# Performance work log

Hardware: AMD Instinct MI355X
Metric: run time of the kernel (lower is better)

## Reference

```python
import jax, jax.numpy as jnp
import numpy as np

B, S, D, H = 4, 2048, 512, 8
HD = D // H


def rotate_half(t):
    half = t.shape[-1] // 2
    return jnp.concatenate([-t[..., half:], t[..., :half]], axis=-1)


def setup_inputs() -> dict:
    key = jax.random.key(0)
    ks = jax.random.split(key, 8)
    x = jax.random.normal(ks[0], (B, S, D), dtype=jnp.float32)
    # realistic rotary tables built from angles
    inv_freq = 1.0 / (10000.0 ** (jnp.arange(0, D // 2, dtype=jnp.float32) / (D // 2)))
    ang = jnp.arange(S, dtype=jnp.float32)[:, None] * inv_freq[None, :]  # [S, D/2]
    ang = jnp.concatenate([ang, ang], axis=-1)  # [S, D]
    cos_emb = jnp.cos(ang)[None]  # [1, S, D]
    sin_emb = jnp.sin(ang)[None]
    mask = jax.random.randint(ks[1], (B, S, S), 0, 2).astype(jnp.bool_)
    scale = 1.0 / np.sqrt(D)
    wq = jax.random.normal(ks[2], (D, D), dtype=jnp.float32) * scale
    wk = jax.random.normal(ks[3], (D, D), dtype=jnp.float32) * scale
    wv = jax.random.normal(ks[4], (D, D), dtype=jnp.float32) * scale
    wo = jax.random.normal(ks[5], (D, D), dtype=jnp.float32) * scale
    return {"x": x, "cos_emb": cos_emb, "sin_emb": sin_emb, "mask": mask,
            "wq": wq, "wk": wk, "wv": wv, "wo": wo}


def reference(x, cos_emb, sin_emb, mask, wq, wk, wv, wo):
    bsz, seqlen, dim = x.shape
    # projections (weights stored as [in, out])
    xq = x @ wq
    xk = x @ wk
    xv = x @ wv
    # RoPE applied over full dim before head split (as in original)
    xq = xq * cos_emb + rotate_half(xq) * sin_emb
    xk = xk * cos_emb + rotate_half(xk) * sin_emb
    # split heads: [B, H, S, HD]
    xq = xq.reshape(bsz, seqlen, H, HD).transpose(0, 2, 1, 3)
    xk = xk.reshape(bsz, seqlen, H, HD).transpose(0, 2, 1, 3)
    xv = xv.reshape(bsz, seqlen, H, HD).transpose(0, 2, 1, 3)
    scores = jnp.einsum('bhqd,bhkd->bhqk', xq, xk) / jnp.sqrt(jnp.float32(HD))
    scores = scores + (~mask)[:, None].astype(scores.dtype) * (-1e9)
    scores = jax.nn.softmax(scores.astype(jnp.float32), axis=-1).astype(xq.dtype)
    scores = scores * mask[:, None].astype(scores.dtype)
    out = jnp.einsum('bhqk,bhkd->bhqd', scores, xv)
    out = out.transpose(0, 2, 1, 3).reshape(bsz, seqlen, dim)
    return out @ wo
```

## Files before the change

kernel.cpp:

```cpp
#include <hip/hip_runtime.h>
#include <hip/hip_bf16.h>

typedef __bf16 bf16x8 __attribute__((ext_vector_type(8)));
typedef float f32x4 __attribute__((ext_vector_type(4)));
typedef short short8 __attribute__((ext_vector_type(8)));

#define MFMA16(a, b, c) __builtin_amdgcn_mfma_f32_16x16x32_bf16((a), (b), (c), 0, 0, 0)

static constexpr int S = 2048;
static constexpr int D = 512;
static constexpr int HD = 64;
static constexpr int KBLK = 64;
#define QSCALE 0.18033688011112042f

typedef __attribute__((address_space(1))) const unsigned int gu32;
typedef __attribute__((address_space(3))) unsigned int lu32;

__device__ __forceinline__ void gll16(const void* g, void* l) {
  __builtin_amdgcn_global_load_lds((gu32*)g, (lu32*)l, 16, 0, 0);
}

__device__ __forceinline__ unsigned short f2b(float f) {
  return __builtin_bit_cast(unsigned short, __float2bfloat16(f));
}
__device__ __forceinline__ float b2f(unsigned short u) {
  return __builtin_bit_cast(float, (unsigned)u << 16);
}

__global__ void maskbits_kernel(const int* __restrict__ m, unsigned long long* __restrict__ bits) {
  int gid = blockIdx.x * 256 + threadIdx.x;
  int lane = threadIdx.x & 63;
  unsigned long long w = __ballot(m[gid] != 0);
  if (lane == 0) bits[gid >> 6] = w;
}

__global__ void cast_x_kernel(const float* __restrict__ x, unsigned short* __restrict__ xb) {
  int idx = blockIdx.x * 256 + threadIdx.x;
  float4 v = ((const float4*)x)[idx];
  ushort4 o;
  o.x = f2b(v.x); o.y = f2b(v.y); o.z = f2b(v.z); o.w = f2b(v.w);
  ((ushort4*)xb)[idx] = o;
}

__global__ void wtrans4_kernel(const float* __restrict__ wq, const float* __restrict__ wk,
                               const float* __restrict__ wv, const float* __restrict__ wo,
                               unsigned short* __restrict__ wqkvT, unsigned short* __restrict__ woT) {
  __shared__ float t[64][65];
  const int z = blockIdx.z;
  const float* w = (z == 0) ? wq : (z == 1) ? wk : (z == 2) ? wv : wo;
  unsigned short* dst = (z < 3) ? wqkvT + (size_t)z * 512 * 512 : woT;
  const int i0 = blockIdx.x * 64, o0 = blockIdx.y * 64;
  for (int it = 0; it < 16; ++it) {
    int idx = it * 256 + threadIdx.x;
    int ii = idx >> 6, oo = idx & 63;
    t[oo][ii] = w[(size_t)(i0 + ii) * 512 + o0 + oo];
  }
  __syncthreads();
  for (int it = 0; it < 16; ++it) {
    int idx = it * 256 + threadIdx.x;
    int oo = idx >> 6, ii = idx & 63;
    dst[(size_t)(o0 + oo) * 512 + i0 + ii] = f2b(t[oo][ii]);
  }
}

__global__ __launch_bounds__(256)
void gemm2(const unsigned short* __restrict__ A, const unsigned short* __restrict__ Bt,
           int M, int N, int K, float* __restrict__ Cf,
           unsigned short* __restrict__ qd, unsigned short* __restrict__ kd,
           unsigned short* __restrict__ vtd, int mode) {
  __shared__ alignas(16) unsigned short lds[2][2][4096];
  const int tid = threadIdx.x;
  const int lane = tid & 63, l15 = lane & 15, lg = lane >> 4;
  const int wave = tid >> 6;
  const int m0 = blockIdx.x * 128, n0 = blockIdx.y * 128;
  const int wm = (wave >> 1) * 64, wn = (wave & 1) * 64;
  const int wbase = wave * 512;
  const int grow = tid >> 2, gcol = (tid & 3) * 8;
  f32x4 acc[4][4] = {};
  const int nt = K / 32;

#define GSTAGE(sb, kk)                                                              \
  do {                                                                              \
    gll16(&A[(size_t)(m0 + grow) * K + (kk) + gcol], &lds[sb][0][wbase]);           \
    gll16(&A[(size_t)(m0 + 64 + grow) * K + (kk) + gcol], &lds[sb][0][2048 + wbase]);\
    gll16(&Bt[(size_t)(n0 + grow) * K + (kk) + gcol], &lds[sb][1][wbase]);          \
    gll16(&Bt[(size_t)(n0 + 64 + grow) * K + (kk) + gcol], &lds[sb][1][2048 + wbase]);\
  } while (0)

  GSTAGE(0, 0);
  asm volatile("s_waitcnt vmcnt(0)" ::: "memory");
  __syncthreads();
  for (int t = 0; t < nt; ++t) {
    const int cur = t & 1;
    if (t + 1 < nt) GSTAGE(cur ^ 1, (t + 1) * 32);
    bf16x8 af[4], bfr[4];
#pragma unroll
    for (int i = 0; i < 4; ++i) {
      af[i]  = *(const bf16x8*)&lds[cur][0][(wm + i * 16 + l15) * 32 + lg * 8];
      bfr[i] = *(const bf16x8*)&lds[cur][1][(wn + i * 16 + l15) * 32 + lg * 8];
    }
    __builtin_amdgcn_s_setprio(1);
#pragma unroll
    for (int i = 0; i < 4; ++i)
#pragma unroll
      for (int j = 0; j < 4; ++j)
        acc[i][j] = MFMA16(af[i], bfr[j], acc[i][j]);
    __builtin_amdgcn_s_setprio(0);
    asm volatile("s_waitcnt vmcnt(0)" ::: "memory");
    __syncthreads();
  }
#undef GSTAGE

  if (mode == 0) {
#pragma unroll
    for (int i = 0; i < 4; ++i)
#pragma unroll
      for (int j = 0; j < 4; ++j)
#pragma unroll
        for (int r = 0; r < 4; ++r)
          Cf[(size_t)(m0 + wm + i * 16 + lg * 4 + r) * N + (n0 + wn + j * 16 + l15)] = acc[i][j][r];
  } else {
    const int sel = n0 >> 9;
    const int nb = (n0 & 511) + wn;
    if (sel < 2) {
      unsigned short* dst = (sel == 0) ? qd : kd;
#pragma unroll
      for (int i = 0; i < 4; ++i)
#pragma unroll
        for (int j = 0; j < 4; ++j)
#pragma unroll
          for (int r = 0; r < 4; ++r) {
            const int m = m0 + wm + i * 16 + lg * 4 + r;
            const int nn = nb + j * 16 + l15;
            dst[(((size_t)(m >> 11) * 8 + (nn >> 6)) * 2048 + (m & 2047)) * 64 + (nn & 63)] =
                f2b(acc[i][j][r]);
          }
    } else {
#pragma unroll
      for (int i = 0; i < 4; ++i)
#pragma unroll
        for (int j = 0; j < 4; ++j)
#pragma unroll
          for (int r = 0; r < 4; ++r) {
            const int m = m0 + wm + i * 16 + lg * 4 + r;
            const int nn = nb + j * 16 + l15;
            vtd[(((size_t)(m >> 11) * 8 + (nn >> 6)) * 64 + (nn & 63)) * 2048 + (m & 2047)] =
                f2b(acc[i][j][r]);
          }
    }
  }
}

__global__ void rope_pair_kernel(const unsigned short* __restrict__ qpre, const unsigned short* __restrict__ kpre,
                                 const float* __restrict__ cose, const float* __restrict__ sine,
                                 unsigned short* __restrict__ qb, unsigned short* __restrict__ kb) {
  const int idx = blockIdx.x * 256 + threadIdx.x;
  const int hd0 = (idx & 7) * 8;
  const int rr = idx >> 3;
  const int b = rr >> 13, h = (rr >> 11) & 3, s = rr & 2047;
  const size_t lo = ((size_t)(b * 8 + h) * 2048 + s) * 64 + hd0;
  const size_t hi = lo + (size_t)4 * 2048 * 64;
  const int d0 = h * 64 + hd0;
  short8 qlo = *(const short8*)&qpre[lo];
  short8 qhi = *(const short8*)&qpre[hi];
  short8 klo = *(const short8*)&kpre[lo];
  short8 khi = *(const short8*)&kpre[hi];
  float4 c0 = *(const float4*)&cose[(size_t)s * 512 + d0];
  float4 c1 = *(const float4*)&cose[(size_t)s * 512 + d0 + 4];
  float4 s0 = *(const float4*)&sine[(size_t)s * 512 + d0];
  float4 s1 = *(const float4*)&sine[(size_t)s * 512 + d0 + 4];
  float cc[8] = {c0.x, c0.y, c0.z, c0.w, c1.x, c1.y, c1.z, c1.w};
  float ss[8] = {s0.x, s0.y, s0.z, s0.w, s1.x, s1.y, s1.z, s1.w};
  short8 qolo, qohi, kolo, kohi;
#pragma unroll
  for (int j = 0; j < 8; ++j) {
    float ql = b2f((unsigned short)qlo[j]), qh = b2f((unsigned short)qhi[j]);
    float kl = b2f((unsigned short)klo[j]), kh = b2f((unsigned short)khi[j]);
    qolo[j] = (short)f2b((ql * cc[j] - qh * ss[j]) * QSCALE);
    qohi[j] = (short)f2b((qh * cc[j] + ql * ss[j]) * QSCALE);
    kolo[j] = (short)f2b(kl * cc[j] - kh * ss[j]);
    kohi[j] = (short)f2b(kh * cc[j] + kl * ss[j]);
  }
  *(short8*)&qb[lo] = qolo;
  *(short8*)&qb[hi] = qohi;
  *(short8*)&kb[lo] = kolo;
  *(short8*)&kb[hi] = kohi;
}

__global__ __launch_bounds__(512)
void flash_kernel(const unsigned short* __restrict__ qb, const unsigned short* __restrict__ kb,
                  const unsigned short* __restrict__ vtb, const unsigned long long* __restrict__ mbits,
                  float* __restrict__ op0, float* __restrict__ op1,
                  float* __restrict__ ls0, float* __restrict__ ls1) {
  __shared__ alignas(16) unsigned short kv[3][2][4096];
  __shared__ alignas(16) f32x4 btab[16];
  const int tid = threadIdx.x;
  const int wave = tid >> 6, lane = tid & 63;
  const int l15 = lane & 15, lg = lane >> 4;
  const int swz = (l15 & 7) << 4;
  const int wgid = blockIdx.x;
  const int slot = wgid >> 3;
  const int bh = (wgid & 7) * 4 + (slot & 3);
  const int rest = slot >> 2;
  const int kh = rest & 1;
  const int q0 = (rest >> 1) * 128 + wave * 16;
  const int b = bh >> 3, h = bh & 7;
  const int kbase = kh * 1024;
  const unsigned short* Q = qb + ((size_t)bh * S + q0) * HD;
  const unsigned short* Kp = kb + (size_t)bh * S * HD;
  const unsigned short* Vt = vtb + (size_t)bh * HD * S;
  const unsigned long long* Mrow = mbits + ((size_t)b * S + q0 + l15) * (S / 64) + kh * 16;
  float* opart = kh ? op1 : op0;
  float* lsum = kh ? ls1 : ls0;

  const int srow = tid >> 3;
  const int scol = ((tid & 7) ^ (srow & 7)) * 8;
  const int ksrow = ((srow & 15) >> 2) * 8 + ((srow >> 4) & 1) * 4 + (srow & 3) + (srow >> 5) * 32;
  const int wbase = wave * 512;

  if (tid < 16) {
    f32x4 e;
    e[0] = (tid & 1) ? 0.f : -300.f;
    e[1] = (tid & 2) ? 0.f : -300.f;
    e[2] = (tid & 4) ? 0.f : -300.f;
    e[3] = (tid & 8) ? 0.f : -300.f;
    btab[tid] = e;
  }

  bf16x8 qf0 = *(const bf16x8*)&Q[l15 * HD + lg * 8];
  bf16x8 qf1 = *(const bf16x8*)&Q[l15 * HD + 32 + lg * 8];
  f32x4 o[4] = {};
  float lpart = 0.f;
  const int lgs8 = lg * 8;

  unsigned long long wA = Mrow[0];
  gll16(&Kp[(size_t)(kbase + ksrow) * HD + scol], &kv[0][0][wbase]);
  gll16(&Vt[(size_t)srow * S + kbase + scol], &kv[0][1][wbase]);
  unsigned long long wB = Mrow[1];
  gll16(&Kp[(size_t)(kbase + 64 + ksrow) * HD + scol], &kv[1][0][wbase]);
  gll16(&Vt[(size_t)srow * S + kbase + 64 + scol], &kv[1][1][wbase]);
  asm volatile("s_waitcnt vmcnt(3) lgkmcnt(0)" ::: "memory");
  __builtin_amdgcn_s_barrier();

  int bi = 0;
  for (int t = 0; t < 16; ++t) {
    unsigned long long wC = 0;
    if (t + 2 < 16) {
      const int kn = kbase + (t + 2) * KBLK;
      const int bn = (bi == 0) ? 2 : bi - 1;
      wC = Mrow[t + 2];
      gll16(&Kp[(size_t)(kn + ksrow) * HD + scol], &kv[bn][0][wbase]);
      gll16(&Vt[(size_t)srow * S + kn + scol], &kv[bn][1][wbase]);
    }
    const char* kbp = (const char*)&kv[bi][0][0];
    const char* vbp = (const char*)&kv[bi][1][0];

    f32x4 sc[4] = {};
    __builtin_amdgcn_s_setprio(1);
#pragma unroll
    for (int n = 0; n < 4; ++n) {
      const int cb = (n * 16 + l15) * 128 + ((lg * 16) ^ swz);
      bf16x8 kf0 = *(const bf16x8*)(kbp + cb);
      bf16x8 kf1 = *(const bf16x8*)(kbp + (cb ^ 64));
      sc[n] = MFMA16(kf0, qf0, sc[n]);
      sc[n] = MFMA16(kf1, qf1, sc[n]);
    }
    __builtin_amdgcn_s_setprio(0);

    f32x4 pv[4];
    {
      const unsigned nib0 = (unsigned)(wA >> (lgs8 + 0)) & 15u;
      const unsigned nib1 = (unsigned)(wA >> (lgs8 + 4)) & 15u;
      const unsigned nib2 = (unsigned)(wA >> (lgs8 + 32)) & 15u;
      const unsigned nib3 = (unsigned)(wA >> (lgs8 + 36)) & 15u;
      const f32x4 b0 = btab[nib0], b1 = btab[nib1], b2 = btab[nib2], b3 = btab[nib3];
#pragma unroll
      for (int r = 0; r < 4; ++r) {
        pv[0][r] = __builtin_amdgcn_exp2f(sc[0][r] + b0[r]);
        pv[1][r] = __builtin_amdgcn_exp2f(sc[1][r] + b1[r]);
        pv[2][r] = __builtin_amdgcn_exp2f(sc[2][r] + b2[r]);
        pv[3][r] = __builtin_amdgcn_exp2f(sc[3][r] + b3[r]);
      }
    }
    f32x4 s4 = (pv[0] + pv[1]) + (pv[2] + pv[3]);
    lpart += (s4[0] + s4[1]) + (s4[2] + s4[3]);

    bf16x8 pf0, pf1;
#pragma unroll
    for (int j = 0; j < 4; ++j) {
      pf0[j]     = (__bf16)pv[0][j];
      pf0[j + 4] = (__bf16)pv[1][j];
      pf1[j]     = (__bf16)pv[2][j];
      pf1[j + 4] = (__bf16)pv[3][j];
    }

    __builtin_amdgcn_s_setprio(1);
#pragma unroll
    for (int n = 0; n < 4; ++n) {
      const int cb = (n * 16 + l15) * 128 + ((lg * 16) ^ swz);
      bf16x8 vf0 = *(const bf16x8*)(vbp + cb);
      bf16x8 vf1 = *(const bf16x8*)(vbp + (cb ^ 64));
      o[n] = MFMA16(pf0, vf0, o[n]);
      o[n] = MFMA16(pf1, vf1, o[n]);
    }
    __builtin_amdgcn_s_setprio(0);

    if (t < 14) { asm volatile("s_waitcnt vmcnt(3)" ::: "memory"); }
    else        { asm volatile("s_waitcnt vmcnt(0)" ::: "memory"); }
    __builtin_amdgcn_s_barrier();
    wA = wB; wB = wC;
    bi = (bi == 2) ? 0 : bi + 1;
  }

  lpart += __shfl_xor(lpart, 16);
  lpart += __shfl_xor(lpart, 32);
  if (lg == 0) lsum[(size_t)bh * S + q0 + l15] = lpart;
#pragma unroll
  for (int r = 0; r < 4; ++r)
#pragma unroll
    for (int n = 0; n < 4; ++n)
      opart[((size_t)(b * S + q0 + lg * 4 + r)) * D + h * HD + n * 16 + l15] = o[n][r];
}

__global__ __launch_bounds__(256)
void gemm_fused(const float* __restrict__ op0, const float* __restrict__ op1,
                const float* __restrict__ ls0, const float* __restrict__ ls1,
                const unsigned short* __restrict__ Bt, float* __restrict__ C) {
  __shared__ alignas(16) unsigned short ldsA[2][2048];
  __shared__ alignas(16) unsigned short ldsB[2][4096];
  __shared__ float invt[512];
  const int tid = threadIdx.x;
  const int lane = tid & 63, l15 = lane & 15, lg = lane >> 4;
  const int wave = tid >> 6;
  const int m0 = blockIdx.x * 64, n0 = blockIdx.y * 128;
  const int wm = (wave >> 1) * 32, wn = (wave & 1) * 64;
  const int wbase = wave * 512;
  const int grow = tid >> 2, gcol = (tid & 3) * 8;
  const int arow = m0 + (tid >> 2);
  const size_t abase = (size_t)arow * 512 + (tid & 3) * 8;
  f32x4 acc[2][4] = {};

  for (int e = tid; e < 512; e += 256) {
    const int row = e >> 3, hh = e & 7;
    const int m = m0 + row;
    const size_t li = ((size_t)((m >> 11) * 8 + hh)) * 2048 + (m & 2047);
    const float l = ls0[li] + ls1[li];
    invt[e] = (l > 0.f) ? 1.f / l : 0.f;
  }

#define BSTAGE(sb, kk)                                                               \
  do {                                                                               \
    gll16(&Bt[(size_t)(n0 + grow) * 512 + (kk) + gcol], &ldsB[sb][wbase]);           \
    gll16(&Bt[(size_t)(n0 + 64 + grow) * 512 + (kk) + gcol], &ldsB[sb][2048 + wbase]);\
  } while (0)

  float4 a0, a1, p0, p1;
#define ALOAD(kk)                                          \
  do {                                                     \
    a0 = *(const float4*)&op0[abase + (kk)];               \
    a1 = *(const float4*)&op0[abase + (kk) + 4];           \
    p0 = *(const float4*)&op1[abase + (kk)];               \
    p1 = *(const float4*)&op1[abase + (kk) + 4];           \
  } while (0)

#define AWRITE(sb, kk)                                                       \
  do {                                                                       \
    const float inv = invt[((tid >> 2) << 3) | ((kk) >> 6)];                 \
    short8 pk;                                                               \
    pk[0] = (short)f2b((a0.x + p0.x) * inv);                                 \
    pk[1] = (short)f2b((a0.y + p0.y) * inv);                                 \
    pk[2] = (short)f2b((a0.z + p0.z) * inv);                                 \
    pk[3] = (short)f2b((a0.w + p0.w) * inv);                                 \
    pk[4] = (short)f2b((a1.x + p1.x) * inv);                                 \
    pk[5] = (short)f2b((a1.y + p1.y) * inv);                                 \
    pk[6] = (short)f2b((a1.z + p1.z) * inv);                                 \
    pk[7] = (short)f2b((a1.w + p1.w) * inv);                                 \
    *(short8*)&ldsA[sb][(tid >> 2) * 32 + (tid & 3) * 8] = pk;               \
  } while (0)

  ALOAD(0);
  BSTAGE(0, 0);
  __syncthreads();
  AWRITE(0, 0);
  __syncthreads();

  for (int t = 0; t < 16; ++t) {
    const int cur = t & 1;
    const bool have = (t + 1 < 16);
    if (have) { ALOAD((t + 1) * 32); BSTAGE(cur ^ 1, (t + 1) * 32); }
    bf16x8 af[2], bfr[4];
#pragma unroll
    for (int i = 0; i < 2; ++i)
      af[i] = *(const bf16x8*)&ldsA[cur][(wm + i * 16 + l15) * 32 + lg * 8];
#pragma unroll
    for (int j = 0; j < 4; ++j)
      bfr[j] = *(const bf16x8*)&ldsB[cur][(wn + j * 16 + l15) * 32 + lg * 8];
    __builtin_amdgcn_s_setprio(1);
#pragma unroll
    for (int i = 0; i < 2; ++i)
#pragma unroll
      for (int j = 0; j < 4; ++j)
        acc[i][j] = MFMA16(af[i], bfr[j], acc[i][j]);
    __builtin_amdgcn_s_setprio(0);
    asm volatile("s_waitcnt vmcnt(0)" ::: "memory");
    __syncthreads();
    if (have) AWRITE(cur ^ 1, (t + 1) * 32);
    __syncthreads();
  }
#undef BSTAGE
#undef ALOAD
#undef AWRITE

#pragma unroll
  for (int i = 0; i < 2; ++i)
#pragma unroll
    for (int j = 0; j < 4; ++j)
#pragma unroll
      for (int r = 0; r < 4; ++r)
        C[(size_t)(m0 + wm + i * 16 + lg * 4 + r) * 512 + (n0 + wn + j * 16 + l15)] = acc[i][j][r];
}

extern "C" void kernel_launch(void* const* d_in, const int* in_sizes, int n_in,
                              void* d_out, int out_size, void* d_ws, size_t ws_size,
                              hipStream_t stream) {
  const float* x = (const float*)d_in[0];
  const float* cose = (const float*)d_in[1];
  const float* sine = (const float*)d_in[2];
  const int* mask = (const int*)d_in[3];
  const float* wq = (const float*)d_in[4];
  const float* wk = (const float*)d_in[5];
  const float* wv = (const float*)d_in[6];
  const float* wo = (const float*)d_in[7];
  float* out = (float*)d_out;
  char* ws = (char*)d_ws;

  unsigned short* xb    = (unsigned short*)(ws);
  unsigned short* wqkvT = (unsigned short*)(ws + 8388608);
  unsigned short* woT   = (unsigned short*)(ws + 9961472);
  unsigned short* qpre  = (unsigned short*)(ws + 10485760);
  unsigned short* kpre  = (unsigned short*)(ws + 18874368);
  unsigned short* qbh   = (unsigned short*)(ws + 35651584);
  unsigned short* kbh   = (unsigned short*)(ws + 44040192);
  unsigned short* vtb   = (unsigned short*)(ws + 52428800);
  unsigned long long* mbits = (unsigned long long*)(ws + 60817408);
  float* op0 = (float*)(ws + 10485760);
  float* op1 = (float*)(ws + 62914560);
  float* ls0 = (float*)(ws + 79691776);
  float* ls1 = (float*)(ws + 79953920);

  maskbits_kernel<<<65536, 256, 0, stream>>>(mask, mbits);
  cast_x_kernel<<<4096, 256, 0, stream>>>(x, xb);
  wtrans4_kernel<<<dim3(8, 8, 4), 256, 0, stream>>>(wq, wk, wv, wo, wqkvT, woT);
  gemm2<<<dim3(64, 12), 256, 0, stream>>>(xb, wqkvT, 8192, 1536, 512, nullptr, qpre, kpre, vtb, 1);
  rope_pair_kernel<<<1024, 256, 0, stream>>>(qpre, kpre, cose, sine, qbh, kbh);
  flash_kernel<<<1024, 512, 0, stream>>>(qbh, kbh, vtb, mbits, op0, op1, ls0, ls1);
  gemm_fused<<<dim3(128, 4), 256, 0, stream>>>(op0, op1, ls0, ls1, woT, out);
}
```

Measured before the change: 131.7 us.

## Stage V-transpose through LDS, grid-stride maskbits, and double-buffer flash K/V

In gemm2, the transposed V output now goes through a padded per-wave LDS tile, so each row is written to global memory with 16-byte coalesced stores instead of scattered 2-byte writes. The maskbits kernel becomes a grid-stride loop over 2048 blocks in place of 65536 blocks, which cuts launch and scheduling overhead. The flash kernel drops from triple to double buffering of K/V with full vmcnt(0) waits and __syncthreads each iteration, lowering LDS use but exposing more load latency. Overall this combines several unrelated changes whose effects may offset one another.

```diff
diff --git a/kernel.cpp b/kernel.cpp
--- a/kernel.cpp
+++ b/kernel.cpp
@@ -28,10 +28,12 @@
 }
 
 __global__ void maskbits_kernel(const int* __restrict__ m, unsigned long long* __restrict__ bits) {
-  int gid = blockIdx.x * 256 + threadIdx.x;
-  int lane = threadIdx.x & 63;
-  unsigned long long w = __ballot(m[gid] != 0);
-  if (lane == 0) bits[gid >> 6] = w;
+  const int stride = 2048 * 256;
+  const int lane0 = (threadIdx.x & 63) == 0;
+  for (int gid = blockIdx.x * 256 + threadIdx.x; gid < 4 * 2048 * 2048; gid += stride) {
+    unsigned long long w = __ballot(m[gid] != 0);
+    if (lane0) bits[gid >> 6] = w;
+  }
 }
 
 __global__ void cast_x_kernel(const float* __restrict__ x, unsigned short* __restrict__ xb) {
@@ -68,7 +70,8 @@
            int M, int N, int K, float* __restrict__ Cf,
            unsigned short* __restrict__ qd, unsigned short* __restrict__ kd,
            unsigned short* __restrict__ vtd, int mode) {
-  __shared__ alignas(16) unsigned short lds[2][2][4096];
+  __shared__ alignas(16) unsigned char smem[36864];
+  unsigned short (*lds)[2][4096] = (unsigned short (*)[2][4096])smem;
   const int tid = threadIdx.x;
   const int lane = tid & 63, l15 = lane & 15, lg = lane >> 4;
   const int wave = tid >> 6;
@@ -136,17 +139,26 @@
                 f2b(acc[i][j][r]);
           }
     } else {
+      unsigned short* tb = (unsigned short*)smem + wave * 4608;
 #pragma unroll
       for (int i = 0; i < 4; ++i)
 #pragma unroll
-        for (int j = 0; j < 4; ++j)
-#pragma unroll
-          for (int r = 0; r < 4; ++r) {
-            const int m = m0 + wm + i * 16 + lg * 4 + r;
-            const int nn = nb + j * 16 + l15;
-            vtd[(((size_t)(m >> 11) * 8 + (nn >> 6)) * 64 + (nn & 63)) * 2048 + (m & 2047)] =
-                f2b(acc[i][j][r]);
-          }
+        for (int j = 0; j < 4; ++j) {
+          ushort4 pk;
+          pk.x = f2b(acc[i][j][0]); pk.y = f2b(acc[i][j][1]);
+          pk.z = f2b(acc[i][j][2]); pk.w = f2b(acc[i][j][3]);
+          *(ushort4*)&tb[(j * 16 + l15) * 72 + i * 16 + lg * 4] = pk;
+        }
+      const int b0 = m0 >> 11;
+      const int s0 = (m0 & 2047) + wm;
+      const int g = lane >> 3, c = lane & 7;
+#pragma unroll
+      for (int rr = 0; rr < 8; ++rr) {
+        const int row = rr * 8 + g;
+        const int nng = nb + row;
+        uint4 v = *(const uint4*)&tb[row * 72 + c * 8];
+        *(uint4*)&vtd[(((size_t)(b0 * 8) + (nng >> 6)) * 64 + (nng & 63)) * 2048 + s0 + c * 8] = v;
+      }
     }
   }
 }
@@ -192,7 +204,7 @@
                   const unsigned short* __restrict__ vtb, const unsigned long long* __restrict__ mbits,
                   float* __restrict__ op0, float* __restrict__ op1,
                   float* __restrict__ ls0, float* __restrict__ ls1) {
-  __shared__ alignas(16) unsigned short kv[3][2][4096];
+  __shared__ alignas(16) unsigned short kv[2][2][4096];
   __shared__ alignas(16) f32x4 btab[16];
   const int tid = threadIdx.x;
   const int wave = tid >> 6, lane = tid & 63;
@@ -236,24 +248,20 @@
   unsigned long long wA = Mrow[0];
   gll16(&Kp[(size_t)(kbase + ksrow) * HD + scol], &kv[0][0][wbase]);
   gll16(&Vt[(size_t)srow * S + kbase + scol], &kv[0][1][wbase]);
-  unsigned long long wB = Mrow[1];
-  gll16(&Kp[(size_t)(kbase + 64 + ksrow) * HD + scol], &kv[1][0][wbase]);
-  gll16(&Vt[(size_t)srow * S + kbase + 64 + scol], &kv[1][1][wbase]);
-  asm volatile("s_waitcnt vmcnt(3) lgkmcnt(0)" ::: "memory");
-  __builtin_amdgcn_s_barrier();
-
-  int bi = 0;
+  asm volatile("s_waitcnt vmcnt(0) lgkmcnt(0)" ::: "memory");
+  __syncthreads();
+
   for (int t = 0; t < 16; ++t) {
-    unsigned long long wC = 0;
-    if (t + 2 < 16) {
-      const int kn = kbase + (t + 2) * KBLK;
-      const int bn = (bi == 0) ? 2 : bi - 1;
-      wC = Mrow[t + 2];
-      gll16(&Kp[(size_t)(kn + ksrow) * HD + scol], &kv[bn][0][wbase]);
-      gll16(&Vt[(size_t)srow * S + kn + scol], &kv[bn][1][wbase]);
-    }
-    const char* kbp = (const char*)&kv[bi][0][0];
-    const char* vbp = (const char*)&kv[bi][1][0];
+    const int cur = t & 1;
+    unsigned long long wB = 0;
+    if (t + 1 < 16) {
+      const int kn = kbase + (t + 1) * KBLK;
+      gll16(&Kp[(size_t)(kn + ksrow) * HD + scol], &kv[cur ^ 1][0][wbase]);
+      gll16(&Vt[(size_t)srow * S + kn + scol], &kv[cur ^ 1][1][wbase]);
+      wB = Mrow[t + 1];
+    }
+    const char* kbp = (const char*)&kv[cur][0][0];
+    const char* vbp = (const char*)&kv[cur][1][0];
 
     f32x4 sc[4] = {};
     __builtin_amdgcn_s_setprio(1);
@@ -269,11 +277,10 @@
 
     f32x4 pv[4];
     {
-      const unsigned nib0 = (unsigned)(wA >> (lgs8 + 0)) & 15u;
-      const unsigned nib1 = (unsigned)(wA >> (lgs8 + 4)) & 15u;
-      const unsigned nib2 = (unsigned)(wA >> (lgs8 + 32)) & 15u;
-      const unsigned nib3 = (unsigned)(wA >> (lgs8 + 36)) & 15u;
-      const f32x4 b0 = btab[nib0], b1 = btab[nib1], b2 = btab[nib2], b3 = btab[nib3];
+      const f32x4 b0 = btab[(unsigned)(wA >> (lgs8 + 0)) & 15u];
+      const f32x4 b1 = btab[(unsigned)(wA >> (lgs8 + 4)) & 15u];
+      const f32x4 b2 = btab[(unsigned)(wA >> (lgs8 + 32)) & 15u];
+      const f32x4 b3 = btab[(unsigned)(wA >> (lgs8 + 36)) & 15u];
 #pragma unroll
       for (int r = 0; r < 4; ++r) {
         pv[0][r] = __builtin_amdgcn_exp2f(sc[0][r] + b0[r]);
@@ -305,11 +312,9 @@
     }
     __builtin_amdgcn_s_setprio(0);
 
-    if (t < 14) { asm volatile("s_waitcnt vmcnt(3)" ::: "memory"); }
-    else        { asm volatile("s_waitcnt vmcnt(0)" ::: "memory"); }
-    __builtin_amdgcn_s_barrier();
-    wA = wB; wB = wC;
-    bi = (bi == 2) ? 0 : bi + 1;
+    asm volatile("s_waitcnt vmcnt(0)" ::: "memory");
+    __syncthreads();
+    wA = wB;
   }
 
   lpart += __shfl_xor(lpart, 16);
@@ -336,8 +341,7 @@
   const int wm = (wave >> 1) * 32, wn = (wave & 1) * 64;
   const int wbase = wave * 512;
   const int grow = tid >> 2, gcol = (tid & 3) * 8;
-  const int arow = m0 + (tid >> 2);
-  const size_t abase = (size_t)arow * 512 + (tid & 3) * 8;
+  const size_t abase = (size_t)(m0 + (tid >> 2)) * 512 + (tid & 3) * 8;
   f32x4 acc[2][4] = {};
 
   for (int e = tid; e < 512; e += 256) {
@@ -448,7 +452,7 @@
   float* ls0 = (float*)(ws + 79691776);
   float* ls1 = (float*)(ws + 79953920);
 
-  maskbits_kernel<<<65536, 256, 0, stream>>>(mask, mbits);
+  maskbits_kernel<<<2048, 256, 0, stream>>>(mask, mbits);
   cast_x_kernel<<<4096, 256, 0, stream>>>(x, xb);
   wtrans4_kernel<<<dim3(8, 8, 4), 256, 0, stream>>>(wq, wk, wv, wo, wqkvT, woT);
   gemm2<<<dim3(64, 12), 256, 0, stream>>>(xb, wqkvT, 8192, 1536, 512, nullptr, qpre, kpre, vtb, 1);
```

Result: faster. 123.0 us (-6.6%).
